# Optimization experiments

Measured on AMD Instinct MI355X. Metric: run time of the kernel, lower is better.

Reference implementation:

```python
import jax, jax.numpy as jnp
import numpy as np

PATCH_SIZE = 3
T = 1.0


def _aggregate_one(v, shift_map, cost_map):
    # v: (C, H, W); shift_map: (2, K, H, W) int; cost_map: (K, H, W)
    p = PATCH_SIZE // 2
    K, H, W = cost_map.shape
    # pad cost with high value (10 -> near-zero softmax weight), shifts with 10 (junk, clamped later)
    pc = jnp.pad(cost_map, ((0, 0), (p, p), (p, p)), constant_values=10.0)
    ps = jnp.pad(shift_map, ((0, 0), (0, 0), (p, p), (p, p)), constant_values=10)
    costs, sis, sjs = [], [], []
    for di in range(PATCH_SIZE):          # small fixed loop (patch_size^2 = 9)
        for dj in range(PATCH_SIZE):
            costs.append(pc[:, di:di + H, dj:dj + W])
            sis.append(ps[0, :, di:di + H, dj:dj + W] + (p - di))
            sjs.append(ps[1, :, di:di + H, dj:dj + W] + (p - dj))
    all_cost = jnp.concatenate(costs, axis=0)                # (P2K, H, W)
    ii = jnp.clip(jnp.concatenate(sis, axis=0), 0, v.shape[1] - 1)
    jj = jnp.clip(jnp.concatenate(sjs, axis=0), 0, v.shape[2] - 1)
    w = jax.nn.softmax(-all_cost / T, axis=0)                # softmax over P2K candidates
    gathered = v[:, ii, jj]                                  # (C, P2K, H, W) irregular gather
    return jnp.sum(w[None] * gathered, axis=1)               # (C, H, W)


def setup_inputs() -> dict:
    key = jax.random.key(0)
    k1, k2, k3 = jax.random.split(key, 3)
    B, C, H, W, K = 2, 32, 256, 256, 4
    v = jax.random.normal(k1, (B, C, H, W), dtype=jnp.float32)
    cost_map = jax.random.uniform(k2, (B, K, H, W), dtype=jnp.float32)
    shift_map = jax.random.randint(k3, (B, 2, K, H, W), 0, H).astype(jnp.int64)
    return {"v": v, "cost_map": cost_map, "shift_map": shift_map}


def reference(v, cost_map, shift_map):
    # Batched PSAttentionMasked.forward with aggregation=True;
    # shift_map/cost_map stand in for the opaque PatchMatch custom kernel output.
    return jax.vmap(_aggregate_one)(v, shift_map, cost_map)
```

## Files before the change

### kernel.cpp

```cpp
#include <hip/hip_runtime.h>
#include <hip/hip_fp16.h>

#define B_ 2
#define C_ 32
#define H_ 256
#define W_ 256
#define K_ 4
#define HW_ (H_ * W_)

__global__ __launch_bounds__(256) void transpose_v_kernel(
    const float* __restrict__ v, unsigned int* __restrict__ vt) {
  __shared__ float tile[32][65];
  int t = threadIdx.x;
  int pix0 = blockIdx.x * 64;
  int b = pix0 >> 16;
  int pixb = pix0 & (HW_ - 1);
  const float* vb = v + (size_t)b * C_ * HW_;
#pragma unroll
  for (int it = 0; it < 8; ++it) {
    int c = (t >> 6) + it * 4;
    int px = t & 63;
    tile[c][px] = __builtin_nontemporal_load(&vb[(size_t)c * HW_ + pixb + px]);
  }
  __syncthreads();
  unsigned int* vtb = vt + (size_t)pix0 * (C_ / 2);
#pragma unroll
  for (int it = 0; it < 4; ++it) {
    int px = (t >> 4) + it * 16;
    int c2 = t & 15;
    float lo = tile[2 * c2][px];
    float hi = tile[2 * c2 + 1][px];
    __half2 h = __floats2half2_rn(lo, hi);
    unsigned int bits;
    __builtin_memcpy(&bits, &h, 4);
    __builtin_nontemporal_store(bits, &vtb[px * 16 + c2]);
  }
}

__global__ __launch_bounds__(256, 3) void psatt_kernel(
    const float* __restrict__ cost_map, const int* __restrict__ shift_map,
    const unsigned int* __restrict__ vt, float* __restrict__ out) {
  __shared__ float2 lds_eo[36][64];
  __shared__ float lds_part[64][4];
  __shared__ float lds_inv[64];
  __shared__ float lds_out[64][33];

  int t = threadIdx.x;
  int bid = blockIdx.x;
  int xcd = bid & 7;
  int slot = bid >> 3;
  int b = xcd >> 2;
  int workid = ((xcd & 3) << 8) + slot;
  int y = workid >> 2;
  int x0 = (workid & 3) << 6;

  {
    int k = t >> 6;
    int px = t & 63;
    int x = x0 + px;
    const float* cm = cost_map + (size_t)(b * K_ + k) * HW_;
    const int* s0 = shift_map + (size_t)((b * 2 + 0) * K_ + k) * HW_;
    const int* s1 = shift_map + (size_t)((b * 2 + 1) * K_ + k) * HW_;
    float psum = 0.f;
#pragma unroll
    for (int di = 0; di < 3; ++di) {
      int ny = y + di - 1;
      bool yin = (unsigned)ny < (unsigned)H_;
#pragma unroll
      for (int dj = 0; dj < 3; ++dj) {
        int nx = x + dj - 1;
        bool inb = yin && ((unsigned)nx < (unsigned)W_);
        int nidx = ny * W_ + nx;
        float cost;
        int si, sj;
        if (inb) {
          cost = cm[nidx];
          si = s0[nidx] + (1 - di);
          sj = s1[nidx] + (1 - dj);
        } else {
          cost = 10.0f;
          si = 11 - di;
          sj = 11 - dj;
        }
        float e = __expf(-cost);
        int ii = min(max(si, 0), H_ - 1);
        int jj = min(max(sj, 0), W_ - 1);
        int m = k * 9 + di * 3 + dj;
        lds_eo[m][px] = make_float2(e, __int_as_float(ii * W_ + jj));
        psum += e;
      }
    }
    lds_part[px][k] = psum;
  }
  __syncthreads();
  if (t < 64) {
    lds_inv[t] =
        1.0f / (lds_part[t][0] + lds_part[t][1] + lds_part[t][2] + lds_part[t][3]);
  }
  __syncthreads();

  {
    int q = t & 3;
    int px = t >> 2;
    const uint4* vbase = (const uint4*)vt + (size_t)b * HW_ * 4 + q;
    float acc[8] = {0.f, 0.f, 0.f, 0.f, 0.f, 0.f, 0.f, 0.f};
#pragma unroll
    for (int half = 0; half < 2; ++half) {
      uint4 hv[18];
      float ew[18];
#pragma unroll
      for (int m = 0; m < 18; ++m) {
        float2 eo = lds_eo[half * 18 + m][px];
        ew[m] = eo.x;
        int off = __float_as_int(eo.y);
        hv[m] = vbase[(size_t)off << 2];
      }
#pragma unroll
      for (int m = 0; m < 18; ++m) {
        float e = ew[m];
        __half2 h0, h1, h2, h3;
        __builtin_memcpy(&h0, &hv[m].x, 4);
        __builtin_memcpy(&h1, &hv[m].y, 4);
        __builtin_memcpy(&h2, &hv[m].z, 4);
        __builtin_memcpy(&h3, &hv[m].w, 4);
        float2 f0 = __half22float2(h0);
        float2 f1 = __half22float2(h1);
        float2 f2 = __half22float2(h2);
        float2 f3 = __half22float2(h3);
        acc[0] += e * f0.x; acc[1] += e * f0.y;
        acc[2] += e * f1.x; acc[3] += e * f1.y;
        acc[4] += e * f2.x; acc[5] += e * f2.y;
        acc[6] += e * f3.x; acc[7] += e * f3.y;
      }
    }
    float inv = lds_inv[px];
#pragma unroll
    for (int j = 0; j < 8; ++j) {
      lds_out[px][8 * q + j] = acc[j] * inv;
    }
  }
  __syncthreads();

  {
    int px = t & 63;
#pragma unroll
    for (int it = 0; it < 8; ++it) {
      int c = (t >> 6) + it * 4;
      __builtin_nontemporal_store(
          lds_out[px][c],
          &out[((size_t)(b * C_ + c) * H_ + y) * W_ + x0 + px]);
    }
  }
}

extern "C" void kernel_launch(void* const* d_in, const int* in_sizes, int n_in,
                              void* d_out, int out_size, void* d_ws, size_t ws_size,
                              hipStream_t stream) {
  const float* v = (const float*)d_in[0];
  const float* cost_map = (const float*)d_in[1];
  const int* shift_map = (const int*)d_in[2];
  float* out = (float*)d_out;

  unsigned int* vt = (unsigned int*)d_ws;
  const int grid = B_ * H_ * (W_ / 64);

  transpose_v_kernel<<<B_ * HW_ / 64, 256, 0, stream>>>(v, vt);
  psatt_kernel<<<grid, 256, 0, stream>>>(cost_map, shift_map, vt, out);
}
```

Baseline: 44.35 us.

## Split gather candidates across lanes with shuffle reduction and vectorize transpose

The transpose kernel now loads v with 16-byte vector loads and writes each pixel's 32 half channels as 16-byte stores. The main kernel changes its work mapping: instead of one pixel per 4 threads looping over 36 candidates, a wavefront processes 4 pixels at a time, with lanes split across (k, dj, channel quarter). Candidate offsets are pre-scaled to bytes and padded to a 4-wide dj slot with zero weight. Partial sums are combined with xor shuffles, which spreads the gather latency across more in-flight lanes and removes one barrier, but adds many shuffles and wasted zero-weight gathers.

```diff
diff --git a/kernel.cpp b/kernel.cpp
--- a/kernel.cpp
+++ b/kernel.cpp
@@ -8,6 +8,9 @@
 #define K_ 4
 #define HW_ (H_ * W_)
 
+typedef float floatx4 __attribute__((ext_vector_type(4)));
+typedef unsigned int uintx4 __attribute__((ext_vector_type(4)));
+
 __global__ __launch_bounds__(256) void transpose_v_kernel(
     const float* __restrict__ v, unsigned int* __restrict__ vt) {
   __shared__ float tile[32][65];
@@ -16,33 +19,36 @@
   int b = pix0 >> 16;
   int pixb = pix0 & (HW_ - 1);
   const float* vb = v + (size_t)b * C_ * HW_;
+  int c = t >> 3;
+  int f = t & 7;
 #pragma unroll
-  for (int it = 0; it < 8; ++it) {
-    int c = (t >> 6) + it * 4;
-    int px = t & 63;
-    tile[c][px] = __builtin_nontemporal_load(&vb[(size_t)c * HW_ + pixb + px]);
+  for (int h = 0; h < 2; ++h) {
+    int px = h * 32 + f * 4;
+    floatx4 r = __builtin_nontemporal_load(
+        (const floatx4*)&vb[(size_t)c * HW_ + pixb + px]);
+    tile[c][px + 0] = r.x;
+    tile[c][px + 1] = r.y;
+    tile[c][px + 2] = r.z;
+    tile[c][px + 3] = r.w;
   }
   __syncthreads();
-  unsigned int* vtb = vt + (size_t)pix0 * (C_ / 2);
-#pragma unroll
-  for (int it = 0; it < 4; ++it) {
-    int px = (t >> 4) + it * 16;
-    int c2 = t & 15;
-    float lo = tile[2 * c2][px];
-    float hi = tile[2 * c2 + 1][px];
-    __half2 h = __floats2half2_rn(lo, hi);
-    unsigned int bits;
-    __builtin_memcpy(&bits, &h, 4);
-    __builtin_nontemporal_store(bits, &vtb[px * 16 + c2]);
-  }
+  int px = t >> 2, q = t & 3;
+  unsigned int w0, w1, w2, w3;
+  { __half2 h2 = __floats2half2_rn(tile[8*q+0][px], tile[8*q+1][px]); __builtin_memcpy(&w0, &h2, 4); }
+  { __half2 h2 = __floats2half2_rn(tile[8*q+2][px], tile[8*q+3][px]); __builtin_memcpy(&w1, &h2, 4); }
+  { __half2 h2 = __floats2half2_rn(tile[8*q+4][px], tile[8*q+5][px]); __builtin_memcpy(&w2, &h2, 4); }
+  { __half2 h2 = __floats2half2_rn(tile[8*q+6][px], tile[8*q+7][px]); __builtin_memcpy(&w3, &h2, 4); }
+  uintx4 o;
+  o.x = w0; o.y = w1; o.z = w2; o.w = w3;
+  __builtin_nontemporal_store(
+      o, (uintx4*)((char*)vt + ((size_t)(pix0 + px) << 6) + (q << 4)));
 }
 
 __global__ __launch_bounds__(256, 3) void psatt_kernel(
     const float* __restrict__ cost_map, const int* __restrict__ shift_map,
     const unsigned int* __restrict__ vt, float* __restrict__ out) {
-  __shared__ float2 lds_eo[36][64];
+  __shared__ float2 lds_ew[64][49];
   __shared__ float lds_part[64][4];
-  __shared__ float lds_inv[64];
   __shared__ float lds_out[64][33];
 
   int t = threadIdx.x;
@@ -85,58 +91,79 @@
         float e = __expf(-cost);
         int ii = min(max(si, 0), H_ - 1);
         int jj = min(max(sj, 0), W_ - 1);
-        int m = k * 9 + di * 3 + dj;
-        lds_eo[m][px] = make_float2(e, __int_as_float(ii * W_ + jj));
+        float offf = __int_as_float((ii * W_ + jj) << 6);
+        lds_ew[px][k * 12 + di * 4 + dj] = make_float2(e, offf);
+        if (dj == 2) {
+          lds_ew[px][k * 12 + di * 4 + 3] = make_float2(0.f, offf);
+        }
         psum += e;
       }
     }
     lds_part[px][k] = psum;
   }
   __syncthreads();
-  if (t < 64) {
-    lds_inv[t] =
-        1.0f / (lds_part[t][0] + lds_part[t][1] + lds_part[t][2] + lds_part[t][3]);
-  }
-  __syncthreads();
 
   {
-    int q = t & 3;
-    int px = t >> 2;
-    const uint4* vbase = (const uint4*)vt + (size_t)b * HW_ * 4 + q;
-    float acc[8] = {0.f, 0.f, 0.f, 0.f, 0.f, 0.f, 0.f, 0.f};
+    int lane = t & 63;
+    int wv = t >> 6;
+    int u = lane >> 4;
+    int dj = (lane >> 2) & 3;
+    int q = lane & 3;
+    const char* base = (const char*)vt + ((size_t)b * HW_ << 6);
+    unsigned int qoff = (unsigned int)(q << 4);
+    int sbase = u * 12 + dj;
+    int jsel = lane >> 2;
+#pragma unroll 1
+    for (int batch = 0; batch < 4; ++batch) {
+      int pxb = (wv << 4) + (batch << 2);
+      uint4 hv[4][3];
+      float ew[4][3];
 #pragma unroll
-    for (int half = 0; half < 2; ++half) {
-      uint4 hv[18];
-      float ew[18];
+      for (int pp = 0; pp < 4; ++pp) {
 #pragma unroll
-      for (int m = 0; m < 18; ++m) {
-        float2 eo = lds_eo[half * 18 + m][px];
-        ew[m] = eo.x;
-        int off = __float_as_int(eo.y);
-        hv[m] = vbase[(size_t)off << 2];
+        for (int di = 0; di < 3; ++di) {
+          float2 eo = lds_ew[pxb + pp][sbase + di * 4];
+          ew[pp][di] = eo.x;
+          unsigned int voff = (unsigned int)__float_as_int(eo.y) + qoff;
+          hv[pp][di] = *(const uint4*)(base + voff);
+        }
       }
 #pragma unroll
-      for (int m = 0; m < 18; ++m) {
-        float e = ew[m];
-        __half2 h0, h1, h2, h3;
-        __builtin_memcpy(&h0, &hv[m].x, 4);
-        __builtin_memcpy(&h1, &hv[m].y, 4);
-        __builtin_memcpy(&h2, &hv[m].z, 4);
-        __builtin_memcpy(&h3, &hv[m].w, 4);
-        float2 f0 = __half22float2(h0);
-        float2 f1 = __half22float2(h1);
-        float2 f2 = __half22float2(h2);
-        float2 f3 = __half22float2(h3);
-        acc[0] += e * f0.x; acc[1] += e * f0.y;
-        acc[2] += e * f1.x; acc[3] += e * f1.y;
-        acc[4] += e * f2.x; acc[5] += e * f2.y;
-        acc[6] += e * f3.x; acc[7] += e * f3.y;
+      for (int pp = 0; pp < 4; ++pp) {
+        int px = pxb + pp;
+        float acc[8] = {0.f, 0.f, 0.f, 0.f, 0.f, 0.f, 0.f, 0.f};
+#pragma unroll
+        for (int di = 0; di < 3; ++di) {
+          float e = ew[pp][di];
+          uint4 hvv = hv[pp][di];
+          __half2 h0, h1, h2, h3;
+          __builtin_memcpy(&h0, &hvv.x, 4);
+          __builtin_memcpy(&h1, &hvv.y, 4);
+          __builtin_memcpy(&h2, &hvv.z, 4);
+          __builtin_memcpy(&h3, &hvv.w, 4);
+          float2 f0 = __half22float2(h0);
+          float2 f1 = __half22float2(h1);
+          float2 f2 = __half22float2(h2);
+          float2 f3 = __half22float2(h3);
+          acc[0] += e * f0.x; acc[1] += e * f0.y;
+          acc[2] += e * f1.x; acc[3] += e * f1.y;
+          acc[4] += e * f2.x; acc[5] += e * f2.y;
+          acc[6] += e * f3.x; acc[7] += e * f3.y;
+        }
+#pragma unroll
+        for (int j = 0; j < 8; ++j) {
+          acc[j] += __shfl_xor(acc[j], 4);
+          acc[j] += __shfl_xor(acc[j], 8);
+          acc[j] += __shfl_xor(acc[j], 16);
+          acc[j] += __shfl_xor(acc[j], 32);
+        }
+        float4 ps = *(const float4*)&lds_part[px][0];
+        float inv = 1.0f / (ps.x + ps.y + ps.z + ps.w);
+        float val = acc[0];
+#pragma unroll
+        for (int j = 1; j < 8; ++j) val = (jsel == j) ? acc[j] : val;
+        if (lane < 32) lds_out[px][(q << 3) + jsel] = val * inv;
       }
-    }
-    float inv = lds_inv[px];
-#pragma unroll
-    for (int j = 0; j < 8; ++j) {
-      lds_out[px][8 * q + j] = acc[j] * inv;
     }
   }
   __syncthreads();
```

After: 68.76 us. 1.55x slower.
